# Kernel optimization log

Measured on AMD Instinct MI355X. Metric: run time of the kernel, lower is better.

## Reference

```python
import jax, jax.numpy as jnp
import numpy as np

E = 8            # num_experts
K = 2            # top-k
CF = 1.25        # capacity_factor
NOISE_STD = 1.0 / E   # noise_mult / num_experts


def setup_inputs() -> dict:
    key = jax.random.key(0)
    ks = jax.random.split(key, 4)
    B, S, D, H = 8, 1024, 768, 3072
    x = jax.random.normal(ks[0], (B, S, D), jnp.float32)
    router_w = jax.random.normal(ks[1], (D, E), jnp.float32) * 0.02
    fc1_w = jax.random.normal(ks[2], (E, D, H), jnp.float32) * 0.02
    fc1_b = jnp.zeros((E, H), jnp.float32)
    fc2_w = jax.random.normal(ks[3], (E, H, D), jnp.float32) * 0.02
    fc2_b = jnp.zeros((E, D), jnp.float32)
    return dict(x=x, router_w=router_w, fc1_w=fc1_w, fc1_b=fc1_b, fc2_w=fc2_w, fc2_b=fc2_b)


def reference(x, router_w, fc1_w, fc1_b, fc2_w, fc2_b):
    B, S, D = x.shape
    N = B * S
    A = N * K                                   # total (token, slot) assignments
    capacity = int(round(K * N * CF / E))
    x_flat = x.reshape(N, D)

    # ---- router (eval mode: no noise, no dropout) ----
    logits = (x_flat @ router_w).astype(jnp.float32)          # [N,E]
    clean_probs = jax.nn.softmax(logits, axis=-1)
    noisy_logits = logits
    noisy_probs = jax.nn.softmax(noisy_logits, axis=-1)
    topk_probs, topk_idx = jax.lax.top_k(noisy_probs, K)      # [N,K]
    topk_probs = topk_probs.astype(x.dtype)

    flat_e = topk_idx.reshape(-1)                             # [A]
    expert_counts = jax.ops.segment_sum(jnp.ones((A,), jnp.float32), flat_e, num_segments=E)

    # ---- aux losses ----
    importance = clean_probs.sum(0)
    mi = importance.mean()
    loss_importance = jnp.var(importance) / (mi * mi + 1e-6)
    # kthvalue(noisy_logits, E-K+1) == (E-K+1)-th smallest == sorted[:, E-K]
    threshold = jnp.sort(noisy_logits, axis=-1)[:, E - K][:, None]
    prob_selected = 1.0 - jax.scipy.stats.norm.cdf(threshold - logits, loc=0.0, scale=NOISE_STD)
    load = prob_selected.sum(0)
    ml = load.mean()
    loss_load = jnp.var(load) / (ml * ml + 1e-6)
    aux_loss = 0.5 * (loss_importance + loss_load)

    # ---- priority-based capacity dropping (vectorized over all assignments) ----
    priority = clean_probs.max(-1)                            # [N]
    tok = jnp.repeat(jnp.arange(N, dtype=jnp.int32), K)       # [A] token of each assignment
    kslot = jnp.tile(jnp.arange(K, dtype=jnp.int32), N)       # [A] which top-k slot
    score = priority[tok] - kslot.astype(jnp.float32)         # combined_scores = -k_idx + priority
    # group by expert (ascending), within expert sort by score descending
    sort_key = flat_e.astype(jnp.float32) * (K + 2) - score
    order = jnp.argsort(sort_key)
    e_sorted = flat_e[order]
    counts = jax.ops.segment_sum(jnp.ones((A,), jnp.int32), flat_e, num_segments=E)
    starts = jnp.cumsum(counts) - counts
    rank_sorted = jnp.arange(A, dtype=jnp.int32) - starts[e_sorted]   # position within expert group
    rank = jnp.zeros((A,), jnp.int32).at[order].set(rank_sorted)
    keep = rank < capacity
    dropped = jnp.sum(~keep).astype(jnp.int32)

    # ---- dispatch into fixed [E, capacity] buffer (overflow slot sliced off) ----
    pos = jnp.where(keep, flat_e * capacity + rank, E * capacity)
    dispatch_tok = jnp.zeros((E * capacity + 1,), jnp.int32).at[pos].set(tok)[:-1]
    w_flat = topk_probs.reshape(-1)
    weight_buf = jnp.zeros((E * capacity + 1,), x.dtype).at[pos].set(jnp.where(keep, w_flat, 0.0))[:-1]

    xe = x_flat[dispatch_tok].reshape(E, capacity, D)         # gather
    h = jax.nn.gelu(jnp.einsum('ecd,edh->ech', xe, fc1_w) + fc1_b[:, None, :], approximate=False)
    ye = jnp.einsum('ech,ehd->ecd', h, fc2_w) + fc2_b[:, None, :]
    weighted = ye * weight_buf.reshape(E, capacity, 1)
    # padded slots have weight 0 and token 0 -> contribute nothing
    out_flat = jnp.zeros((N, D), x.dtype).at[dispatch_tok].add(weighted.reshape(E * capacity, D))

    return out_flat.reshape(B, S, D), aux_loss, dropped, expert_counts
```

## Files before the change

### kernel.cpp

```cpp
#include <hip/hip_runtime.h>
#include <hip/hip_bf16.h>
#include <math.h>

#define NTOK 8192
#define DIM  768
#define HDIM 3072
#define NE   8
#define CAP  2560
#define AMAX 16384

typedef __bf16 bf16x8  __attribute__((ext_vector_type(8)));
typedef __bf16 bf16x2  __attribute__((ext_vector_type(2)));
typedef float  floatx4 __attribute__((ext_vector_type(4)));

typedef unsigned int u32_g __attribute__((address_space(1)));
typedef unsigned int u32_l __attribute__((address_space(3)));

__device__ __forceinline__ void gl_lds16(const void* g, void* l) {
  __builtin_amdgcn_global_load_lds((const u32_g*)g, (u32_l*)l, 16, 0, 0);
}

__device__ __forceinline__ float gelu_exact(float v) {
  float z = fabsf(v) * 0.7071067811865475f;
  float t = __builtin_amdgcn_rcpf(1.0f + 0.3275911f * z);
  float p = ((((1.061405429f * t - 1.453152027f) * t + 1.421413741f) * t
              - 0.284496736f) * t + 0.254829592f) * t;
  float e = 1.0f - p * __expf(-z * z);
  e = copysignf(e, v);
  return 0.5f * v * (1.0f + e);
}

__global__ __launch_bounds__(256) void transpose_conv2(
    const float* __restrict__ w1, const float* __restrict__ w2,
    __bf16* __restrict__ o1, __bf16* __restrict__ o2)
{
  const int which = blockIdx.z;
  const float* src = which ? w2 : w1;
  __bf16* dst = which ? o2 : o1;
  const int Kd = which ? HDIM : DIM;
  const int Nd = which ? DIM : HDIM;
  const int e = blockIdx.y;
  const int tilesK = Kd >> 6;
  const int bk = blockIdx.x % tilesK, bn = blockIdx.x / tilesK;
  __shared__ float T[64][65];
  const float* se = src + (size_t)e * Kd * Nd;
  const int k0 = bk * 64, n0 = bn * 64;
  const int tid = threadIdx.x;
#pragma unroll
  for (int it = 0; it < 16; ++it) {
    int flat = tid + it * 256;
    int kk = flat >> 6, nn = flat & 63;
    T[kk][nn] = se[(size_t)(k0 + kk) * Nd + n0 + nn];
  }
  __syncthreads();
  const int n = tid >> 2, kg = tid & 3;
  bf16x8 v0, v1;
#pragma unroll
  for (int q = 0; q < 8; ++q) v0[q] = (__bf16)T[kg * 16 + q][n];
#pragma unroll
  for (int q = 0; q < 8; ++q) v1[q] = (__bf16)T[kg * 16 + 8 + q][n];
  __bf16* de = dst + (size_t)e * Nd * Kd + (size_t)(n0 + n) * Kd + k0 + kg * 16;
  *(bf16x8*)(de) = v0;
  *(bf16x8*)(de + 8) = v1;
}

__global__ __launch_bounds__(256) void router_kernel(
    const float* __restrict__ x, const float* __restrict__ rw,
    int* __restrict__ list_len, double* __restrict__ imp, double* __restrict__ loadacc,
    int* __restrict__ aidx, float* __restrict__ keyarr, float* __restrict__ warr)
{
  __shared__ float Wl[NE * DIM];
  __shared__ int   lcount[NE], lbase[NE];
  __shared__ int   s_e[32][2], s_pos[32][2];
  __shared__ float s_key[32][2], s_w[32][2];
  const int tid = threadIdx.x;
  for (int i = tid; i < NE * DIM; i += 256) {
    int e = i / DIM, d = i - e * DIM;
    Wl[i] = rw[d * NE + e];
  }
  if (tid < NE) lcount[tid] = 0;
  __syncthreads();
  const int wave = tid >> 6, lane = tid & 63;
  double my_imp = 0.0, my_load = 0.0;

  for (int it = 0; it < 8; ++it) {
    const int t = wave * 8 + it;
    const int n = blockIdx.x * 32 + t;
    const float* xr = x + (size_t)n * DIM;
    float part[NE];
#pragma unroll
    for (int e = 0; e < NE; ++e) part[e] = 0.f;
#pragma unroll
    for (int c = 0; c < DIM / 64; ++c) {
      float xv = xr[c * 64 + lane];
#pragma unroll
      for (int e = 0; e < NE; ++e) part[e] += xv * Wl[e * DIM + c * 64 + lane];
    }
#pragma unroll
    for (int off = 32; off > 0; off >>= 1) {
#pragma unroll
      for (int e = 0; e < NE; ++e) part[e] += __shfl_xor(part[e], off);
    }
    int e0 = 0; float v0 = part[0];
#pragma unroll
    for (int e = 1; e < NE; ++e) if (part[e] > v0) { v0 = part[e]; e0 = e; }
    int e1 = -1; float v1 = -3.4e38f;
#pragma unroll
    for (int e = 0; e < NE; ++e) if (e != e0 && part[e] > v1) { v1 = part[e]; e1 = e; }

    float pexp[NE]; float s = 0.f;
#pragma unroll
    for (int e = 0; e < NE; ++e) { pexp[e] = expf(part[e] - v0); s += pexp[e]; }
    const float inv = 1.0f / s;
    const float pr = inv;
    float w1v = 0.f;
#pragma unroll
    for (int e = 0; e < NE; ++e) if (e == e1) w1v = pexp[e] * inv;

    float myl = 0.f, mypexp = 0.f;
#pragma unroll
    for (int e = 0; e < NE; ++e) if (lane == e) { myl = part[e]; mypexp = pexp[e]; }
    if (lane < NE) {
      my_imp  += (double)(mypexp * inv);
      my_load += (double)(0.5f * erfcf((v1 - myl) * 5.656854249492380f));
    }
    if (lane == 0) {
      int p0 = atomicAdd(&lcount[e0], 1);
      int p1 = atomicAdd(&lcount[e1], 1);
      s_e[t][0] = e0; s_pos[t][0] = p0;
      s_key[t][0] = (float)(e0 * 4) - pr;
      s_w[t][0] = pr;
      s_e[t][1] = e1; s_pos[t][1] = p1;
      s_key[t][1] = (float)(e1 * 4) - (pr - 1.0f);
      s_w[t][1] = w1v;
    }
  }
  __syncthreads();
  if (tid < NE) lbase[tid] = atomicAdd(&list_len[tid], lcount[tid]);
  __syncthreads();
  if (tid < 64) {
    const int t = tid >> 1, sl = tid & 1;
    const int e = s_e[t][sl];
    const int gp = lbase[e] + s_pos[t][sl];
    const int n = blockIdx.x * 32 + t;
    aidx[e * AMAX + gp]   = n * 2 + sl;
    keyarr[e * AMAX + gp] = s_key[t][sl];
    warr[e * AMAX + gp]   = s_w[t][sl];
  }
  if (lane < NE) {
    unsafeAtomicAdd(&imp[lane], my_imp);
    unsafeAtomicAdd(&loadacc[lane], my_load);
  }
}

__global__ __launch_bounds__(256) void compact_kernel(
    const int* __restrict__ list_len, const int* __restrict__ aidx,
    const float* __restrict__ keyarr, const float* __restrict__ warr,
    int* __restrict__ dtok, float* __restrict__ dw,
    const double* __restrict__ imp, const double* __restrict__ loadacc,
    float* __restrict__ out_scalars)
{
  __shared__ float sk[6144];
  __shared__ int   sa[6144];
  const int e = blockIdx.x, tid = threadIdx.x;
  const int C = list_len[e];
  if (C <= CAP) {
    for (int t = tid; t < C; t += 256) {
      int a = aidx[e * AMAX + t];
      dtok[e * CAP + t] = a >> 1;
      dw[e * CAP + t]   = warr[e * AMAX + t];
    }
  } else {
    const bool useL = (C <= 6144);
    if (useL) {
      for (int t = tid; t < C; t += 256) { sk[t] = keyarr[e*AMAX+t]; sa[t] = aidx[e*AMAX+t]; }
      __syncthreads();
    }
    for (int t = tid; t < C; t += 256) {
      float kt = keyarr[e*AMAX+t]; int at = aidx[e*AMAX+t];
      int r = 0;
      for (int u = 0; u < C; ++u) {
        float ku = useL ? sk[u] : keyarr[e*AMAX+u];
        int   au = useL ? sa[u] : aidx[e*AMAX+u];
        if (ku < kt || (ku == kt && au < at)) ++r;
      }
      if (r < CAP) { dtok[e*CAP + r] = at >> 1; dw[e*CAP + r] = warr[e*AMAX+t]; }
    }
  }
  if (e == 0 && tid == 0) {
    double mi = 0, ml = 0;
    for (int i = 0; i < NE; ++i) { mi += imp[i]; ml += loadacc[i]; }
    mi /= NE; ml /= NE;
    double vi = 0, vl = 0;
    for (int i = 0; i < NE; ++i) {
      double di = imp[i] - mi;     vi += di * di;
      double dl = loadacc[i] - ml; vl += dl * dl;
    }
    vi /= NE; vl /= NE;
    double li = vi / (mi * mi + 1e-6), ll = vl / (ml * ml + 1e-6);
    out_scalars[0] = (float)(0.5 * (li + ll));
    int drop = 0;
    for (int i = 0; i < NE; ++i) { int c2 = list_len[i]; if (c2 > CAP) drop += c2 - CAP; }
    out_scalars[1] = (float)drop;
    for (int i = 0; i < NE; ++i) out_scalars[2 + i] = (float)list_len[i];
  }
}

__global__ __launch_bounds__(256) void gather_kernel(
    const float* __restrict__ x, const int* __restrict__ dtok,
    const int* __restrict__ list_len, __bf16* __restrict__ Ag)
{
  const int row  = blockIdx.x * 4 + (threadIdx.x >> 6);
  const int lane = threadIdx.x & 63;
  const int e = row / CAP, slot = row - e * CAP;
  const int kept = min(list_len[e], CAP);
  __bf16* dst = Ag + (size_t)row * DIM;
  if (slot < kept) {
    const float* srcr = x + (size_t)dtok[e * CAP + slot] * DIM;
#pragma unroll
    for (int c = 0; c < DIM / 128; ++c) {
      float2 v = *(const float2*)(srcr + c * 128 + lane * 2);
      bf16x2 o; o[0] = (__bf16)v.x; o[1] = (__bf16)v.y;
      *(bf16x2*)(dst + c * 128 + lane * 2) = o;
    }
  } else {
    bf16x2 z; z[0] = (__bf16)0.f; z[1] = (__bf16)0.f;
#pragma unroll
    for (int c = 0; c < DIM / 128; ++c) *(bf16x2*)(dst + c * 128 + lane * 2) = z;
  }
}

template<int MODE>
__global__ __launch_bounds__(256, 2) void moe_gemm(
    const __bf16* __restrict__ Aall, const __bf16* __restrict__ BTall,
    const float* __restrict__ bias, __bf16* __restrict__ Hout,
    float* __restrict__ Out, const int* __restrict__ dtok, const float* __restrict__ dww,
    const int* __restrict__ list_len, int Kd, int Nd, int tilesM)
{
  const int i_blk = blockIdx.x;
  const int xcd = i_blk & 7, q = i_blk >> 3;
  const int e = xcd;
  const int tm = q % tilesM;
  int tn, ks, kbase, kIters;
  if (MODE == 0) {
    tn = q / tilesM; ks = 0; kbase = 0; kIters = Kd >> 5;
  } else {
    const int pr = q / tilesM;
    tn = pr % 3; ks = pr / 3; kbase = ks * (Kd >> 1); kIters = Kd >> 6;
  }

  const int kept = min(list_len[e], CAP);
  const int mUsed = (kept + 127) >> 7;
  if (tm >= mUsed) return;

  __shared__ __bf16 S[3][12288];

  const int tid = threadIdx.x, lane = tid & 63, wave = tid >> 6;
  const int wm = wave & 1, wn = wave >> 1;
  const int m0 = tm * 128, n0 = tn * 256;

  const __bf16* Ae = Aall + (size_t)e * CAP * Kd + kbase;
  const __bf16* Be = BTall + (size_t)e * Nd * Kd + kbase;

  const int lr = lane & 15, lc = (lane >> 4) * 8;
  const __bf16* gA[2]; const __bf16* gB[4];
  int sAo[2], sBo[4];
#pragma unroll
  for (int a = 0; a < 2; ++a) {
    const int g = wave * 2 + a;
    gA[a] = Ae + (size_t)(m0 + g * 16 + lr) * Kd + lc;
    sAo[a] = g * 512;
  }
#pragma unroll
  for (int b = 0; b < 4; ++b) {
    const int h = wave * 4 + b;
    gB[b] = Be + (size_t)(n0 + h * 16 + lr) * Kd + lc;
    sBo[b] = 4096 + h * 512;
  }

  floatx4 acc[4][8];
#pragma unroll
  for (int i = 0; i < 4; ++i)
#pragma unroll
    for (int j = 0; j < 8; ++j) acc[i][j] = (floatx4)0.f;

#define ISSUE(J, Bf)                                           \
  do {                                                         \
    const int _off = (J) * 32;                                 \
    gl_lds16(gA[0] + _off, &S[(Bf)][sAo[0]]);                  \
    gl_lds16(gA[1] + _off, &S[(Bf)][sAo[1]]);                  \
    gl_lds16(gB[0] + _off, &S[(Bf)][sBo[0]]);                  \
    gl_lds16(gB[1] + _off, &S[(Bf)][sBo[1]]);                  \
    gl_lds16(gB[2] + _off, &S[(Bf)][sBo[2]]);                  \
    gl_lds16(gB[3] + _off, &S[(Bf)][sBo[3]]);                  \
  } while (0)

  ISSUE(0, 0);
  ISSUE(1, 1);
  int cur = 0;
  for (int kt = 0; kt < kIters; ++kt) {
    if (kt < kIters - 1) __builtin_amdgcn_s_waitcnt(0x0F76);
    else                 __builtin_amdgcn_s_waitcnt(0x0F70);
    asm volatile("" ::: "memory");
    __builtin_amdgcn_s_barrier();
    asm volatile("" ::: "memory");

    bf16x8 af[4], bfr[8];
#pragma unroll
    for (int i = 0; i < 4; ++i)
      af[i]  = *(const bf16x8*)(&S[cur][((wm * 4 + i) * 64 + lane) * 8]);
#pragma unroll
    for (int j = 0; j < 8; ++j)
      bfr[j] = *(const bf16x8*)(&S[cur][4096 + ((wn * 8 + j) * 64 + lane) * 8]);

    if (kt + 2 < kIters) {
      int nb = cur + 2; if (nb >= 3) nb -= 3;
      ISSUE(kt + 2, nb);
    }

#pragma unroll
    for (int i = 0; i < 4; ++i)
#pragma unroll
      for (int j = 0; j < 8; ++j)
        acc[i][j] = __builtin_amdgcn_mfma_f32_16x16x32_bf16(af[i], bfr[j], acc[i][j], 0, 0, 0);

    cur = (cur == 2) ? 0 : cur + 1;
  }
#undef ISSUE

  const int quad = lane >> 4, lcol = lane & 15;
  float bcol[8];
#pragma unroll
  for (int j = 0; j < 8; ++j)
    bcol[j] = (MODE == 1 && ks == 1) ? 0.f : bias[e * Nd + n0 + wn * 128 + j * 16 + lcol];

  if (MODE == 0) {
#pragma unroll
    for (int i = 0; i < 4; ++i) {
#pragma unroll
      for (int r = 0; r < 4; ++r) {
        const int row = m0 + wm * 64 + i * 16 + quad * 4 + r;
        __bf16* hrow = Hout + ((size_t)(e * CAP + row)) * Nd;
#pragma unroll
        for (int j = 0; j < 8; ++j) {
          float v = acc[i][j][r] + bcol[j];
          hrow[n0 + wn * 128 + j * 16 + lcol] = (__bf16)gelu_exact(v);
        }
      }
    }
  } else {
#pragma unroll
    for (int i = 0; i < 4; ++i) {
#pragma unroll
      for (int r = 0; r < 4; ++r) {
        const int row = m0 + wm * 64 + i * 16 + quad * 4 + r;
        const float w = dww[e * CAP + row];
        if (w != 0.0f) {
          const int tok = dtok[e * CAP + row];
          float* orow = Out + (size_t)tok * DIM;
#pragma unroll
          for (int j = 0; j < 8; ++j) {
            float v = w * (acc[i][j][r] + bcol[j]);
            unsafeAtomicAdd(&orow[n0 + wn * 128 + j * 16 + lcol], v);
          }
        }
      }
    }
  }
}

extern "C" void kernel_launch(void* const* d_in, const int* in_sizes, int n_in,
                              void* d_out, int out_size, void* d_ws, size_t ws_size,
                              hipStream_t stream) {
  (void)in_sizes; (void)n_in; (void)out_size; (void)ws_size;
  const float* x  = (const float*)d_in[0];
  const float* rw = (const float*)d_in[1];
  const float* w1 = (const float*)d_in[2];
  const float* b1 = (const float*)d_in[3];
  const float* w2 = (const float*)d_in[4];
  const float* b2 = (const float*)d_in[5];
  float* out = (float*)d_out;
  char* ws = (char*)d_ws;

  int*    list_len = (int*)(ws + 0);
  double* imp      = (double*)(ws + 64);
  double* loadacc  = (double*)(ws + 128);
  int*    dtok     = (int*)(ws + 256);
  float*  dw       = (float*)(ws + 256 + 81920);
  int*    aidx     = (int*)(ws + 164096);
  float*  keyarr   = (float*)(ws + 164096 + 524288);
  float*  warr     = (float*)(ws + 164096 + 1048576);
  __bf16* W1T      = (__bf16*)(ws + 2097152);
  __bf16* W2T      = (__bf16*)(ws + 2097152 + 37748736);
  __bf16* Ag       = (__bf16*)(ws + 2097152 + 2 * 37748736);
  __bf16* hbuf     = (__bf16*)(ws + 2097152 + 2 * 37748736 + 31457280);

  hipMemsetAsync(d_out, 0, (size_t)NTOK * DIM * sizeof(float), stream);
  hipMemsetAsync(ws, 0, 164096, stream);

  transpose_conv2<<<dim3(576, 8, 2), 256, 0, stream>>>(w1, w2, W1T, W2T);
  router_kernel<<<NTOK / 32, 256, 0, stream>>>(x, rw, list_len, imp, loadacc, aidx, keyarr, warr);
  compact_kernel<<<NE, 256, 0, stream>>>(list_len, aidx, keyarr, warr, dtok, dw, imp, loadacc,
                                         out + (size_t)NTOK * DIM);
  gather_kernel<<<(NE * CAP) / 4, 256, 0, stream>>>(x, dtok, list_len, Ag);
  moe_gemm<0><<<NE * 20 * (HDIM / 256), 256, 0, stream>>>(
      Ag, W1T, b1, hbuf, nullptr, nullptr, nullptr, list_len, DIM, HDIM, 20);
  moe_gemm<1><<<NE * 20 * (DIM / 256) * 2, 256, 0, stream>>>(
      hbuf, W2T, b2, nullptr, out, dtok, dw, list_len, HDIM, DIM, 20);
}
```

Measured before the change: 579.2 us.

## Replace LDS-staged GEMM tiles with direct register-prefetched global loads

The expert GEMM kernel no longer stages A/B tiles through a triple-buffered shared-memory pipeline with barriers. Each wave now loads its own MFMA fragments directly from global memory into registers, double-buffered across K iterations. This removes LDS traffic and block-wide barriers, but gives up cross-wave tile sharing, which increases global/L2 load volume and register usage.

```diff
diff --git a/kernel.cpp b/kernel.cpp
--- a/kernel.cpp
+++ b/kernel.cpp
@@ -12,13 +12,6 @@
 typedef __bf16 bf16x8  __attribute__((ext_vector_type(8)));
 typedef __bf16 bf16x2  __attribute__((ext_vector_type(2)));
 typedef float  floatx4 __attribute__((ext_vector_type(4)));
-
-typedef unsigned int u32_g __attribute__((address_space(1)));
-typedef unsigned int u32_l __attribute__((address_space(3)));
-
-__device__ __forceinline__ void gl_lds16(const void* g, void* l) {
-  __builtin_amdgcn_global_load_lds((const u32_g*)g, (u32_l*)l, 16, 0, 0);
-}
 
 __device__ __forceinline__ float gelu_exact(float v) {
   float z = fabsf(v) * 0.7071067811865475f;
@@ -253,30 +246,20 @@
   const int mUsed = (kept + 127) >> 7;
   if (tm >= mUsed) return;
 
-  __shared__ __bf16 S[3][12288];
-
   const int tid = threadIdx.x, lane = tid & 63, wave = tid >> 6;
   const int wm = wave & 1, wn = wave >> 1;
-  const int m0 = tm * 128, n0 = tn * 256;
+  const int m0 = tm * 128 + wm * 64;
+  const int n0 = tn * 256 + wn * 128;
 
   const __bf16* Ae = Aall + (size_t)e * CAP * Kd + kbase;
   const __bf16* Be = BTall + (size_t)e * Nd * Kd + kbase;
 
   const int lr = lane & 15, lc = (lane >> 4) * 8;
-  const __bf16* gA[2]; const __bf16* gB[4];
-  int sAo[2], sBo[4];
-#pragma unroll
-  for (int a = 0; a < 2; ++a) {
-    const int g = wave * 2 + a;
-    gA[a] = Ae + (size_t)(m0 + g * 16 + lr) * Kd + lc;
-    sAo[a] = g * 512;
-  }
-#pragma unroll
-  for (int b = 0; b < 4; ++b) {
-    const int h = wave * 4 + b;
-    gB[b] = Be + (size_t)(n0 + h * 16 + lr) * Kd + lc;
-    sBo[b] = 4096 + h * 512;
-  }
+  const __bf16* pA[4]; const __bf16* pB[8];
+#pragma unroll
+  for (int i = 0; i < 4; ++i) pA[i] = Ae + (size_t)(m0 + i * 16 + lr) * Kd + lc;
+#pragma unroll
+  for (int j = 0; j < 8; ++j) pB[j] = Be + (size_t)(n0 + j * 16 + lr) * Kd + lc;
 
   floatx4 acc[4][8];
 #pragma unroll
@@ -284,67 +267,59 @@
 #pragma unroll
     for (int j = 0; j < 8; ++j) acc[i][j] = (floatx4)0.f;
 
-#define ISSUE(J, Bf)                                           \
-  do {                                                         \
-    const int _off = (J) * 32;                                 \
-    gl_lds16(gA[0] + _off, &S[(Bf)][sAo[0]]);                  \
-    gl_lds16(gA[1] + _off, &S[(Bf)][sAo[1]]);                  \
-    gl_lds16(gB[0] + _off, &S[(Bf)][sBo[0]]);                  \
-    gl_lds16(gB[1] + _off, &S[(Bf)][sBo[1]]);                  \
-    gl_lds16(gB[2] + _off, &S[(Bf)][sBo[2]]);                  \
-    gl_lds16(gB[3] + _off, &S[(Bf)][sBo[3]]);                  \
-  } while (0)
-
-  ISSUE(0, 0);
-  ISSUE(1, 1);
-  int cur = 0;
-  for (int kt = 0; kt < kIters; ++kt) {
-    if (kt < kIters - 1) __builtin_amdgcn_s_waitcnt(0x0F76);
-    else                 __builtin_amdgcn_s_waitcnt(0x0F70);
-    asm volatile("" ::: "memory");
-    __builtin_amdgcn_s_barrier();
-    asm volatile("" ::: "memory");
-
-    bf16x8 af[4], bfr[8];
+  bf16x8 a0[4], b0[8], a1[4], b1[8];
+#pragma unroll
+  for (int i = 0; i < 4; ++i) a0[i] = *(const bf16x8*)(pA[i]);
+#pragma unroll
+  for (int j = 0; j < 8; ++j) b0[j] = *(const bf16x8*)(pB[j]);
+
+  for (int kt = 0; kt < kIters; kt += 2) {
+    const int off1 = (kt + 1) * 32;
+    if (kt + 1 < kIters) {
+#pragma unroll
+      for (int i = 0; i < 4; ++i) a1[i] = *(const bf16x8*)(pA[i] + off1);
+#pragma unroll
+      for (int j = 0; j < 8; ++j) b1[j] = *(const bf16x8*)(pB[j] + off1);
+    }
 #pragma unroll
     for (int i = 0; i < 4; ++i)
-      af[i]  = *(const bf16x8*)(&S[cur][((wm * 4 + i) * 64 + lane) * 8]);
-#pragma unroll
-    for (int j = 0; j < 8; ++j)
-      bfr[j] = *(const bf16x8*)(&S[cur][4096 + ((wn * 8 + j) * 64 + lane) * 8]);
-
+#pragma unroll
+      for (int j = 0; j < 8; ++j)
+        acc[i][j] = __builtin_amdgcn_mfma_f32_16x16x32_bf16(a0[i], b0[j], acc[i][j], 0, 0, 0);
+
+    const int off2 = (kt + 2) * 32;
     if (kt + 2 < kIters) {
-      int nb = cur + 2; if (nb >= 3) nb -= 3;
-      ISSUE(kt + 2, nb);
-    }
-
-#pragma unroll
-    for (int i = 0; i < 4; ++i)
-#pragma unroll
-      for (int j = 0; j < 8; ++j)
-        acc[i][j] = __builtin_amdgcn_mfma_f32_16x16x32_bf16(af[i], bfr[j], acc[i][j], 0, 0, 0);
-
-    cur = (cur == 2) ? 0 : cur + 1;
-  }
-#undef ISSUE
+#pragma unroll
+      for (int i = 0; i < 4; ++i) a0[i] = *(const bf16x8*)(pA[i] + off2);
+#pragma unroll
+      for (int j = 0; j < 8; ++j) b0[j] = *(const bf16x8*)(pB[j] + off2);
+    }
+    if (kt + 1 < kIters) {
+#pragma unroll
+      for (int i = 0; i < 4; ++i)
+#pragma unroll
+        for (int j = 0; j < 8; ++j)
+          acc[i][j] = __builtin_amdgcn_mfma_f32_16x16x32_bf16(a1[i], b1[j], acc[i][j], 0, 0, 0);
+    }
+  }
 
   const int quad = lane >> 4, lcol = lane & 15;
   float bcol[8];
 #pragma unroll
   for (int j = 0; j < 8; ++j)
-    bcol[j] = (MODE == 1 && ks == 1) ? 0.f : bias[e * Nd + n0 + wn * 128 + j * 16 + lcol];
+    bcol[j] = (MODE == 1 && ks == 1) ? 0.f : bias[e * Nd + n0 + j * 16 + lcol];
 
   if (MODE == 0) {
 #pragma unroll
     for (int i = 0; i < 4; ++i) {
 #pragma unroll
       for (int r = 0; r < 4; ++r) {
-        const int row = m0 + wm * 64 + i * 16 + quad * 4 + r;
+        const int row = m0 + i * 16 + quad * 4 + r;
         __bf16* hrow = Hout + ((size_t)(e * CAP + row)) * Nd;
 #pragma unroll
         for (int j = 0; j < 8; ++j) {
           float v = acc[i][j][r] + bcol[j];
-          hrow[n0 + wn * 128 + j * 16 + lcol] = (__bf16)gelu_exact(v);
+          hrow[n0 + j * 16 + lcol] = (__bf16)gelu_exact(v);
         }
       }
     }
@@ -353,7 +328,7 @@
     for (int i = 0; i < 4; ++i) {
 #pragma unroll
       for (int r = 0; r < 4; ++r) {
-        const int row = m0 + wm * 64 + i * 16 + quad * 4 + r;
+        const int row = m0 + i * 16 + quad * 4 + r;
         const float w = dww[e * CAP + row];
         if (w != 0.0f) {
           const int tok = dtok[e * CAP + row];
@@ -361,7 +336,7 @@
 #pragma unroll
           for (int j = 0; j < 8; ++j) {
             float v = w * (acc[i][j][r] + bcol[j]);
-            unsafeAtomicAdd(&orow[n0 + wn * 128 + j * 16 + lcol], v);
+            unsafeAtomicAdd(&orow[n0 + j * 16 + lcol], v);
           }
         }
       }
```

Result: slower. 1.242 ms (+114.5%).
